# Optimization experiments

Measured on AMD Instinct MI355X. Metric: run time of the kernel, lower is better.

Reference implementation:

```python
import jax, jax.numpy as jnp
import numpy as np

K = 3; STRIDE = 1; PAD = 1; DIL = 1  # from init_kwargs, groups=1


def setup_inputs() -> dict:
    key = jax.random.key(0)
    k1, k2, k3, k4, k5 = jax.random.split(key, 5)
    x = jax.random.normal(k1, (4, 64, 128, 128), dtype=jnp.float32)
    # small offset-conv weights so predicted offsets stay in a realistic few-pixel range
    w_off = jax.random.normal(k2, (2 * K * K, 64, K, K), dtype=jnp.float32) * 0.01
    b_off = jax.random.normal(k3, (2 * K * K,), dtype=jnp.float32) * 0.01
    w = jax.random.normal(k4, (64, 64, K, K), dtype=jnp.float32) * (1.0 / np.sqrt(64 * K * K))
    b = jax.random.normal(k5, (64,), dtype=jnp.float32) * 0.01
    return {"x": x, "w_off": w_off, "b_off": b_off, "w": w, "b": b}


def _conv2d(x, w, b):
    out = jax.lax.conv_general_dilated(
        x, w, window_strides=(STRIDE, STRIDE), padding=((PAD, PAD), (PAD, PAD)),
        rhs_dilation=(DIL, DIL), dimension_numbers=("NCHW", "OIHW", "NCHW"))
    return out + b[None, :, None, None]


def _deform_sample(x, oy, ox):
    # x: [B,C,H,W]; oy/ox: [B,K2,Ho,Wo] learned offsets (y,x)
    B, C, H, W = x.shape
    K2, Ho, Wo = oy.shape[1], oy.shape[2], oy.shape[3]
    k_idx = jnp.arange(K2)
    kh = (k_idx // K).astype(jnp.float32)
    kw = (k_idx % K).astype(jnp.float32)
    base_y = kh[:, None] * DIL + (jnp.arange(Ho, dtype=jnp.float32) * STRIDE - PAD)[None, :]  # [K2,Ho]
    base_x = kw[:, None] * DIL + (jnp.arange(Wo, dtype=jnp.float32) * STRIDE - PAD)[None, :]  # [K2,Wo]
    y = base_y[None, :, :, None] + oy  # [B,K2,Ho,Wo]
    xp = base_x[None, :, None, :] + ox
    y0f = jnp.floor(y); x0f = jnp.floor(xp)
    wy = y - y0f; wx = xp - x0f
    y0 = y0f.astype(jnp.int32); x0 = x0f.astype(jnp.int32)
    imgf = x.reshape(B, C, H * W)
    N = K2 * Ho * Wo

    def gather(yi, xi, cw):
        valid = (yi >= 0) & (yi < H) & (xi >= 0) & (xi < W)  # zero padding outside
        yc = jnp.clip(yi, 0, H - 1); xc = jnp.clip(xi, 0, W - 1)
        idx = (yc * W + xc).reshape(B, 1, N)
        g = jnp.take_along_axis(imgf, idx, axis=2)  # [B,C,N]
        m = (cw * valid.astype(cw.dtype)).reshape(B, 1, N)
        return g * m

    acc = gather(y0, x0, (1 - wy) * (1 - wx))
    acc = acc + gather(y0, x0 + 1, (1 - wy) * wx)
    acc = acc + gather(y0 + 1, x0, wy * (1 - wx))
    acc = acc + gather(y0 + 1, x0 + 1, wy * wx)
    return acc.reshape(B, C, K2, Ho, Wo)


def reference(x, w_off, b_off, w, b):
    # offset-predicting conv (standard conv2d)
    off = _conv2d(x, w_off, b_off)  # [B, 2*K*K, Ho, Wo]
    B = off.shape[0]; Ho, Wo = off.shape[2], off.shape[3]
    off = off.reshape(B, K * K, 2, Ho, Wo)
    oy, ox = off[:, :, 0], off[:, :, 1]
    sampled = _deform_sample(x, oy, ox)  # [B,C,K2,Ho,Wo]
    O = w.shape[0]
    out = jnp.einsum("bckhw,ock->bohw", sampled, w.reshape(O, w.shape[1], K * K))
    return out + b[None, :, None, None]
```

## Files before the change

### kernel.cpp

```cpp
#include <hip/hip_runtime.h>


typedef unsigned short u16;
typedef __attribute__((ext_vector_type(8))) short bf16x8;
typedef __attribute__((ext_vector_type(4))) float f32x4;
#define MFMA __builtin_amdgcn_mfma_f32_16x16x32_bf16

__device__ __forceinline__ void bsplit(float v, u16& h, u16& l) {
  unsigned u = __float_as_uint(v);
  unsigned hb = (u + 0x7fffu + ((u >> 16) & 1u)) & 0xffff0000u;
  h = (u16)(hb >> 16);
  float r = v - __uint_as_float(hb);
  unsigned u2 = __float_as_uint(r);
  l = (u16)((u2 + 0x7fffu + ((u2 >> 16) & 1u)) >> 16);
}

__device__ __forceinline__ u16 brnd(float v) {
  unsigned u = __float_as_uint(v);
  return (u16)((u + 0x7fffu + ((u >> 16) & 1u)) >> 16);
}

__global__ __launch_bounds__(256) void prep_weights(
    const float* __restrict__ w, const float* __restrict__ w_off,
    u16* __restrict__ whi, u16* __restrict__ wlo,
    u16* __restrict__ wofh, u16* __restrict__ wofl) {
  int t = blockIdx.x * 256 + threadIdx.x;
  int stride = gridDim.x * 256;
  for (int i = t; i < 9 * 64 * 64; i += stride) {
    int tap = i >> 12, o = (i >> 6) & 63, c = i & 63;
    u16 h, l;
    bsplit(w[o * 576 + c * 9 + tap], h, l);
    whi[i] = h; wlo[i] = l;
  }
  for (int i = t; i < 9 * 32 * 64; i += stride) {
    int tap = i >> 11, ch = (i >> 6) & 31, c = i & 63;
    float v = (ch < 18) ? w_off[ch * 576 + c * 9 + tap] : 0.f;
    u16 h, l;
    bsplit(v, h, l);
    wofh[i] = h; wofl[i] = l;
  }
}

__global__ __launch_bounds__(256) void transpose_x(
    const float* __restrict__ x, float* __restrict__ xt) {
  __shared__ float tile[64][65];
  int blk = blockIdx.x;
  int wchunk = blk & 1;
  int h = (blk >> 1) & 127;
  int b = blk >> 8;
  int w0 = wchunk * 64;
  int r = threadIdx.x >> 6;
  int lane = threadIdx.x & 63;
#pragma unroll
  for (int i = 0; i < 16; i++) {
    int c = r + i * 4;
    tile[c][lane] = x[(((size_t)(b * 64 + c) * 128) + h) * 128 + w0 + lane];
  }
  __syncthreads();
#pragma unroll
  for (int i = 0; i < 16; i++) {
    int wi = r + i * 4;
    xt[(((size_t)(b * 128 + h) * 128) + w0 + wi) * 64 + lane] = tile[lane][wi];
  }
}

__global__ __launch_bounds__(256) void offset_conv(
    const float* __restrict__ xt, const u16* __restrict__ wofh,
    const u16* __restrict__ wofl, const float* __restrict__ b_off,
    float* __restrict__ off_pix) {
  int blk = blockIdx.x;
  int h = blk & 127, b = blk >> 7;
  int lane = threadIdx.x & 63, wv = threadIdx.x >> 6;
  int lm = lane & 15, lg = lane >> 4;
  const float* xb = xt + (size_t)b * (128 * 128 * 64);

  f32x4 acc[2][2];
#pragma unroll
  for (int i = 0; i < 2; i++)
#pragma unroll
    for (int j = 0; j < 2; j++) acc[i][j] = (f32x4)0.f;

#pragma unroll 1
  for (int tap = 0; tap < 9; tap++) {
    int ky = tap / 3, kx = tap - ky * 3;
    int y = h + ky - 1;
    if ((unsigned)y >= 128u) continue;
#pragma unroll
    for (int kc = 0; kc < 2; kc++) {
      const u16* ah = wofh + tap * 2048 + lm * 64 + kc * 32 + lg * 8;
      const u16* al = wofl + tap * 2048 + lm * 64 + kc * 32 + lg * 8;
      bf16x8 a0h = *(const bf16x8*)ah;
      bf16x8 a0l = *(const bf16x8*)al;
      bf16x8 a1h = *(const bf16x8*)(ah + 1024);
      bf16x8 a1l = *(const bf16x8*)(al + 1024);
#pragma unroll
      for (int pt = 0; pt < 2; pt++) {
        int xx = wv * 32 + pt * 16 + lm + kx - 1;
        bool valid = (unsigned)xx < 128u;
        int xc = min(max(xx, 0), 127);
        const float* xp = xb + ((size_t)(y * 128 + xc)) * 64 + kc * 32 + lg * 8;
        float4 xa = *(const float4*)xp;
        float4 xd = *(const float4*)(xp + 4);
        if (!valid) { xa = make_float4(0, 0, 0, 0); xd = make_float4(0, 0, 0, 0); }
        bf16x8 bh;
        bh[0] = brnd(xa.x); bh[1] = brnd(xa.y);
        bh[2] = brnd(xa.z); bh[3] = brnd(xa.w);
        bh[4] = brnd(xd.x); bh[5] = brnd(xd.y);
        bh[6] = brnd(xd.z); bh[7] = brnd(xd.w);
        acc[pt][0] = MFMA(a0h, bh, acc[pt][0], 0, 0, 0);
        acc[pt][0] = MFMA(a0l, bh, acc[pt][0], 0, 0, 0);
        acc[pt][1] = MFMA(a1h, bh, acc[pt][1], 0, 0, 0);
        acc[pt][1] = MFMA(a1l, bh, acc[pt][1], 0, 0, 0);
      }
    }
  }

  float4 bo = *(const float4*)(b_off + 4 * lg);
  float b16 = b_off[16], b17 = b_off[17];
#pragma unroll
  for (int pt = 0; pt < 2; pt++) {
    int wc = wv * 32 + pt * 16 + lm;
    size_t base = ((size_t)((b * 128 + h) * 128) + wc) * 18;
    float2 s0 = make_float2(acc[pt][0][0] + bo.x, acc[pt][0][1] + bo.y);
    float2 s1 = make_float2(acc[pt][0][2] + bo.z, acc[pt][0][3] + bo.w);
    *(float2*)(off_pix + base + 4 * lg) = s0;
    *(float2*)(off_pix + base + 4 * lg + 2) = s1;
    if (lg == 0) {
      float2 s2 = make_float2(acc[pt][1][0] + b16, acc[pt][1][1] + b17);
      *(float2*)(off_pix + base + 16) = s2;
    }
  }
}

#define SWZ(p, byt) ((byt) ^ (((p) & 7) << 4))
__global__ __launch_bounds__(256) void dcn_main(
    const float* __restrict__ xt, const float* __restrict__ off_pix,
    const u16* __restrict__ whi, const u16* __restrict__ wlo,
    const float* __restrict__ bias, float* __restrict__ out) {
  __shared__ __align__(16) float cw_lds[576][4];
  __shared__ __align__(16) int   ci_lds[576][4];
  __shared__ __align__(16) u16 shi[64 * 64];

  int blk = blockIdx.x;
  int wg = ((blk & 7) << 7) | (blk >> 3);
  int wc = wg & 1, h = (wg >> 1) & 127, b = wg >> 8;
  int w0 = wc * 64;
  int tid = threadIdx.x, lane = tid & 63, wave = tid >> 6;
  int lm = lane & 15, lg = lane >> 4;
  const float* xbase = xt + (size_t)b * (128 * 128 * 64);
  const float* offbase = off_pix + (size_t)((b * 128 + h) * 128 + w0) * 18;

#pragma unroll 1
  for (int it = tid; it < 576; it += 256) {
    int p = it / 9, k = it - p * 9;
    int ky = k / 3, kx = k - ky * 3;
    float2 o2 = *reinterpret_cast<const float2*>(offbase + p * 18 + 2 * k);
    float yf = (float)(h + ky - 1) + o2.x;
    float xf = (float)(w0 + p + kx - 1) + o2.y;
    float y0f = floorf(yf), x0f = floorf(xf);
    float wy = yf - y0f, wx = xf - x0f;
    int y0 = (int)y0f, x0 = (int)x0f;
    int y1 = y0 + 1, x1 = x0 + 1;
    float w00 = (1.f - wy) * (1.f - wx);
    float w01 = (1.f - wy) * wx;
    float w10 = wy * (1.f - wx);
    float w11 = wy * wx;
    bool vy0 = (unsigned)y0 < 128u, vy1 = (unsigned)y1 < 128u;
    bool vx0 = (unsigned)x0 < 128u, vx1 = (unsigned)x1 < 128u;
    if (!(vy0 && vx0)) w00 = 0.f;
    if (!(vy0 && vx1)) w01 = 0.f;
    if (!(vy1 && vx0)) w10 = 0.f;
    if (!(vy1 && vx1)) w11 = 0.f;
    int y0c = min(max(y0, 0), 127), y1c = min(max(y1, 0), 127);
    int x0c = min(max(x0, 0), 127), x1c = min(max(x1, 0), 127);
    *(float4*)cw_lds[it] = make_float4(w00, w01, w10, w11);
    *(int4*)ci_lds[it] =
        make_int4((y0c * 128 + x0c) * 64, (y0c * 128 + x1c) * 64,
                  (y1c * 128 + x0c) * 64, (y1c * 128 + x1c) * 64);
  }
  __syncthreads();

  f32x4 acc[4];
#pragma unroll
  for (int i = 0; i < 4; i++) acc[i] = (f32x4)0.f;

  float g[16][4];

#pragma unroll
  for (int i = 0; i < 16; i++) {
    int4 ci = *(const int4*)ci_lds[(wave * 16 + i) * 9 + 0];
    g[i][0] = xbase[ci.x + lane];
    g[i][1] = xbase[ci.y + lane];
    g[i][2] = xbase[ci.z + lane];
    g[i][3] = xbase[ci.w + lane];
  }

#pragma unroll 1
  for (int tap = 0; tap < 9; tap++) {
#pragma unroll
    for (int i = 0; i < 16; i++) {
      int p = wave * 16 + i;
      float4 cwv = *(const float4*)cw_lds[p * 9 + tap];
      float v = cwv.x * g[i][0] + cwv.y * g[i][1] +
                cwv.z * g[i][2] + cwv.w * g[i][3];
      int byt = SWZ(p, p * 128 + lane * 2);
      *(u16*)((char*)shi + byt) = brnd(v);
    }
    __syncthreads();

    if (tap < 8) {
#pragma unroll
      for (int i = 0; i < 16; i++) {
        int4 ci = *(const int4*)ci_lds[(wave * 16 + i) * 9 + tap + 1];
        g[i][0] = xbase[ci.x + lane];
        g[i][1] = xbase[ci.y + lane];
        g[i][2] = xbase[ci.z + lane];
        g[i][3] = xbase[ci.w + lane];
      }
    }

    const u16* wh = whi + tap * 4096 + (wave * 16 + lm) * 64 + lg * 8;
    const u16* wl = wlo + tap * 4096 + (wave * 16 + lm) * 64 + lg * 8;
    bf16x8 ah0 = *(const bf16x8*)wh;
    bf16x8 ah1 = *(const bf16x8*)(wh + 32);
    bf16x8 al0 = *(const bf16x8*)wl;
    bf16x8 al1 = *(const bf16x8*)(wl + 32);
#pragma unroll
    for (int pt = 0; pt < 4; pt++) {
      int p = pt * 16 + lm;
      int byt0 = SWZ(p, p * 128 + lg * 16);
      int byt1 = SWZ(p, p * 128 + 64 + lg * 16);
      bf16x8 bh0 = *(const bf16x8*)((char*)shi + byt0);
      bf16x8 bh1 = *(const bf16x8*)((char*)shi + byt1);
      acc[pt] = MFMA(ah0, bh0, acc[pt], 0, 0, 0);
      acc[pt] = MFMA(al0, bh0, acc[pt], 0, 0, 0);
      acc[pt] = MFMA(ah1, bh1, acc[pt], 0, 0, 0);
      acc[pt] = MFMA(al1, bh1, acc[pt], 0, 0, 0);
    }
    __syncthreads();
  }

  float4 bv = *(const float4*)(bias + wave * 16 + 4 * lg);
  size_t ob = ((size_t)(b * 64 + wave * 16 + 4 * lg)) * 16384 + h * 128 + w0;
#pragma unroll
  for (int pt = 0; pt < 4; pt++) {
#pragma unroll
    for (int r = 0; r < 4; r++) {
      float bb = (r == 0) ? bv.x : (r == 1) ? bv.y : (r == 2) ? bv.z : bv.w;
      out[ob + (size_t)r * 16384 + pt * 16 + lm] = acc[pt][r] + bb;
    }
  }
}

extern "C" void kernel_launch(void* const* d_in, const int* in_sizes, int n_in,
                              void* d_out, int out_size, void* d_ws, size_t ws_size,
                              hipStream_t stream) {
  const float* x     = (const float*)d_in[0];
  const float* w_off = (const float*)d_in[1];
  const float* b_off = (const float*)d_in[2];
  const float* w     = (const float*)d_in[3];
  const float* b     = (const float*)d_in[4];
  float* out = (float*)d_out;
  char* ws = (char*)d_ws;

  u16*   whi     = (u16*)(ws);
  u16*   wlo     = (u16*)(ws + 73728);
  u16*   wofh    = (u16*)(ws + 147456);
  u16*   wofl    = (u16*)(ws + 184320);
  float* xtw     = (float*)(ws + 221184);
  float* off_pix = (float*)(ws + 16998400);

  prep_weights<<<64, 256, 0, stream>>>(w, w_off, whi, wlo, wofh, wofl);
  transpose_x<<<1024, 256, 0, stream>>>(x, xtw);
  offset_conv<<<512, 256, 0, stream>>>(xtw, wofh, wofl, b_off, off_pix);
  dcn_main<<<1024, 256, 0, stream>>>(xtw, off_pix, whi, wlo, b, out);
}
```

Before: 169.1 us.

## Fuse offset conv into deformable main kernel and merge prep with transpose

Moves the offset-predicting convolution into the main deformable-conv kernel: each workgroup computes the offsets for its 64 pixels with MFMA and keeps them in LDS instead of writing them to and reading them back from global memory. Weight preparation and the x transpose are merged into one launch, so the pipeline goes from four kernel launches to two. The cost is more LDS and registers per workgroup in the main kernel, which may lower occupancy, plus a serial offset phase ahead of sampling inside each block.

```diff
diff --git a/kernel.cpp b/kernel.cpp
--- a/kernel.cpp
+++ b/kernel.cpp
@@ -20,85 +20,89 @@
   return (u16)((u + 0x7fffu + ((u >> 16) & 1u)) >> 16);
 }
 
-__global__ __launch_bounds__(256) void prep_weights(
-    const float* __restrict__ w, const float* __restrict__ w_off,
+__global__ __launch_bounds__(256) void prep_and_transpose(
+    const float* __restrict__ x, const float* __restrict__ w,
+    const float* __restrict__ w_off, float* __restrict__ xt,
     u16* __restrict__ whi, u16* __restrict__ wlo,
     u16* __restrict__ wofh, u16* __restrict__ wofl) {
-  int t = blockIdx.x * 256 + threadIdx.x;
-  int stride = gridDim.x * 256;
-  for (int i = t; i < 9 * 64 * 64; i += stride) {
-    int tap = i >> 12, o = (i >> 6) & 63, c = i & 63;
-    u16 h, l;
-    bsplit(w[o * 576 + c * 9 + tap], h, l);
-    whi[i] = h; wlo[i] = l;
-  }
-  for (int i = t; i < 9 * 32 * 64; i += stride) {
-    int tap = i >> 11, ch = (i >> 6) & 31, c = i & 63;
-    float v = (ch < 18) ? w_off[ch * 576 + c * 9 + tap] : 0.f;
-    u16 h, l;
-    bsplit(v, h, l);
-    wofh[i] = h; wofl[i] = l;
-  }
-}
-
-__global__ __launch_bounds__(256) void transpose_x(
-    const float* __restrict__ x, float* __restrict__ xt) {
   __shared__ float tile[64][65];
   int blk = blockIdx.x;
-  int wchunk = blk & 1;
-  int h = (blk >> 1) & 127;
-  int b = blk >> 8;
-  int w0 = wchunk * 64;
-  int r = threadIdx.x >> 6;
-  int lane = threadIdx.x & 63;
-#pragma unroll
-  for (int i = 0; i < 16; i++) {
-    int c = r + i * 4;
-    tile[c][lane] = x[(((size_t)(b * 64 + c) * 128) + h) * 128 + w0 + lane];
-  }
-  __syncthreads();
-#pragma unroll
-  for (int i = 0; i < 16; i++) {
-    int wi = r + i * 4;
-    xt[(((size_t)(b * 128 + h) * 128) + w0 + wi) * 64 + lane] = tile[lane][wi];
-  }
-}
-
-__global__ __launch_bounds__(256) void offset_conv(
-    const float* __restrict__ xt, const u16* __restrict__ wofh,
-    const u16* __restrict__ wofl, const float* __restrict__ b_off,
-    float* __restrict__ off_pix) {
+  if (blk < 1024) {
+    int wchunk = blk & 1;
+    int h = (blk >> 1) & 127;
+    int b = blk >> 8;
+    int w0 = wchunk * 64;
+    int r = threadIdx.x >> 6;
+    int lane = threadIdx.x & 63;
+#pragma unroll
+    for (int i = 0; i < 16; i++) {
+      int c = r + i * 4;
+      tile[c][lane] = x[(((size_t)(b * 64 + c) * 128) + h) * 128 + w0 + lane];
+    }
+    __syncthreads();
+#pragma unroll
+    for (int i = 0; i < 16; i++) {
+      int wi = r + i * 4;
+      xt[(((size_t)(b * 128 + h) * 128) + w0 + wi) * 64 + lane] = tile[lane][wi];
+    }
+  } else {
+    int t = (blk - 1024) * 256 + threadIdx.x;
+    const int stride = 64 * 256;
+    for (int i = t; i < 9 * 64 * 64; i += stride) {
+      int tap = i >> 12, o = (i >> 6) & 63, c = i & 63;
+      u16 h, l;
+      bsplit(w[o * 576 + c * 9 + tap], h, l);
+      whi[i] = h; wlo[i] = l;
+    }
+    for (int i = t; i < 9 * 32 * 64; i += stride) {
+      int tap = i >> 11, ch = (i >> 6) & 31, c = i & 63;
+      float v = (ch < 18) ? w_off[ch * 576 + c * 9 + tap] : 0.f;
+      u16 h, l;
+      bsplit(v, h, l);
+      wofh[i] = h; wofl[i] = l;
+    }
+  }
+}
+
+#define SWZ(p, byt) ((byt) ^ (((p) & 7) << 4))
+__global__ __launch_bounds__(256) void dcn_fused(
+    const float* __restrict__ xt,
+    const u16* __restrict__ whi, const u16* __restrict__ wlo,
+    const u16* __restrict__ wofh, const u16* __restrict__ wofl,
+    const float* __restrict__ b_off, const float* __restrict__ bias,
+    float* __restrict__ out) {
+  __shared__ __align__(16) float cw_lds[576][4];
+  __shared__ __align__(16) int   ci_lds[576][4];
+  __shared__ __align__(16) u16   shi[64 * 64];
+  __shared__ __align__(16) float offs[64][20];
+
   int blk = blockIdx.x;
-  int h = blk & 127, b = blk >> 7;
-  int lane = threadIdx.x & 63, wv = threadIdx.x >> 6;
+  int wg = ((blk & 7) << 7) | (blk >> 3);
+  int wc = wg & 1, h = (wg >> 1) & 127, b = wg >> 8;
+  int w0 = wc * 64;
+  int tid = threadIdx.x, lane = tid & 63, wave = tid >> 6;
   int lm = lane & 15, lg = lane >> 4;
-  const float* xb = xt + (size_t)b * (128 * 128 * 64);
-
-  f32x4 acc[2][2];
-#pragma unroll
-  for (int i = 0; i < 2; i++)
-#pragma unroll
-    for (int j = 0; j < 2; j++) acc[i][j] = (f32x4)0.f;
-
+  const float* xbase = xt + (size_t)b * (128 * 128 * 64);
+
+  {
+    f32x4 oa0 = (f32x4)0.f, oa1 = (f32x4)0.f;
 #pragma unroll 1
-  for (int tap = 0; tap < 9; tap++) {
-    int ky = tap / 3, kx = tap - ky * 3;
-    int y = h + ky - 1;
-    if ((unsigned)y >= 128u) continue;
-#pragma unroll
-    for (int kc = 0; kc < 2; kc++) {
-      const u16* ah = wofh + tap * 2048 + lm * 64 + kc * 32 + lg * 8;
-      const u16* al = wofl + tap * 2048 + lm * 64 + kc * 32 + lg * 8;
-      bf16x8 a0h = *(const bf16x8*)ah;
-      bf16x8 a0l = *(const bf16x8*)al;
-      bf16x8 a1h = *(const bf16x8*)(ah + 1024);
-      bf16x8 a1l = *(const bf16x8*)(al + 1024);
-#pragma unroll
-      for (int pt = 0; pt < 2; pt++) {
-        int xx = wv * 32 + pt * 16 + lm + kx - 1;
+    for (int tap = 0; tap < 9; tap++) {
+      int ky = tap / 3, kx = tap - ky * 3;
+      int y = h + ky - 1;
+      if ((unsigned)y >= 128u) continue;
+#pragma unroll
+      for (int kc = 0; kc < 2; kc++) {
+        const u16* ah = wofh + tap * 2048 + lm * 64 + kc * 32 + lg * 8;
+        const u16* al = wofl + tap * 2048 + lm * 64 + kc * 32 + lg * 8;
+        bf16x8 a0h = *(const bf16x8*)ah;
+        bf16x8 a0l = *(const bf16x8*)al;
+        bf16x8 a1h = *(const bf16x8*)(ah + 1024);
+        bf16x8 a1l = *(const bf16x8*)(al + 1024);
+        int xx = w0 + wave * 16 + lm + kx - 1;
         bool valid = (unsigned)xx < 128u;
-        int xc = min(max(xx, 0), 127);
-        const float* xp = xb + ((size_t)(y * 128 + xc)) * 64 + kc * 32 + lg * 8;
+        int xcl = min(max(xx, 0), 127);
+        const float* xp = xbase + ((size_t)(y * 128 + xcl)) * 64 + kc * 32 + lg * 8;
         float4 xa = *(const float4*)xp;
         float4 xd = *(const float4*)(xp + 4);
         if (!valid) { xa = make_float4(0, 0, 0, 0); xd = make_float4(0, 0, 0, 0); }
@@ -107,56 +111,33 @@
         bh[2] = brnd(xa.z); bh[3] = brnd(xa.w);
         bh[4] = brnd(xd.x); bh[5] = brnd(xd.y);
         bh[6] = brnd(xd.z); bh[7] = brnd(xd.w);
-        acc[pt][0] = MFMA(a0h, bh, acc[pt][0], 0, 0, 0);
-        acc[pt][0] = MFMA(a0l, bh, acc[pt][0], 0, 0, 0);
-        acc[pt][1] = MFMA(a1h, bh, acc[pt][1], 0, 0, 0);
-        acc[pt][1] = MFMA(a1l, bh, acc[pt][1], 0, 0, 0);
+        oa0 = MFMA(a0h, bh, oa0, 0, 0, 0);
+        oa0 = MFMA(a0l, bh, oa0, 0, 0, 0);
+        oa1 = MFMA(a1h, bh, oa1, 0, 0, 0);
+        oa1 = MFMA(a1l, bh, oa1, 0, 0, 0);
       }
     }
-  }
-
-  float4 bo = *(const float4*)(b_off + 4 * lg);
-  float b16 = b_off[16], b17 = b_off[17];
-#pragma unroll
-  for (int pt = 0; pt < 2; pt++) {
-    int wc = wv * 32 + pt * 16 + lm;
-    size_t base = ((size_t)((b * 128 + h) * 128) + wc) * 18;
-    float2 s0 = make_float2(acc[pt][0][0] + bo.x, acc[pt][0][1] + bo.y);
-    float2 s1 = make_float2(acc[pt][0][2] + bo.z, acc[pt][0][3] + bo.w);
-    *(float2*)(off_pix + base + 4 * lg) = s0;
-    *(float2*)(off_pix + base + 4 * lg + 2) = s1;
+    int px = wave * 16 + lm;
+    float4 bo = *(const float4*)(b_off + 4 * lg);
+    offs[px][4 * lg + 0] = oa0[0] + bo.x;
+    offs[px][4 * lg + 1] = oa0[1] + bo.y;
+    offs[px][4 * lg + 2] = oa0[2] + bo.z;
+    offs[px][4 * lg + 3] = oa0[3] + bo.w;
     if (lg == 0) {
-      float2 s2 = make_float2(acc[pt][1][0] + b16, acc[pt][1][1] + b17);
-      *(float2*)(off_pix + base + 16) = s2;
-    }
-  }
-}
-
-#define SWZ(p, byt) ((byt) ^ (((p) & 7) << 4))
-__global__ __launch_bounds__(256) void dcn_main(
-    const float* __restrict__ xt, const float* __restrict__ off_pix,
-    const u16* __restrict__ whi, const u16* __restrict__ wlo,
-    const float* __restrict__ bias, float* __restrict__ out) {
-  __shared__ __align__(16) float cw_lds[576][4];
-  __shared__ __align__(16) int   ci_lds[576][4];
-  __shared__ __align__(16) u16 shi[64 * 64];
-
-  int blk = blockIdx.x;
-  int wg = ((blk & 7) << 7) | (blk >> 3);
-  int wc = wg & 1, h = (wg >> 1) & 127, b = wg >> 8;
-  int w0 = wc * 64;
-  int tid = threadIdx.x, lane = tid & 63, wave = tid >> 6;
-  int lm = lane & 15, lg = lane >> 4;
-  const float* xbase = xt + (size_t)b * (128 * 128 * 64);
-  const float* offbase = off_pix + (size_t)((b * 128 + h) * 128 + w0) * 18;
+      offs[px][16] = oa1[0] + b_off[16];
+      offs[px][17] = oa1[1] + b_off[17];
+    }
+  }
+  __syncthreads();
 
 #pragma unroll 1
   for (int it = tid; it < 576; it += 256) {
     int p = it / 9, k = it - p * 9;
     int ky = k / 3, kx = k - ky * 3;
-    float2 o2 = *reinterpret_cast<const float2*>(offbase + p * 18 + 2 * k);
-    float yf = (float)(h + ky - 1) + o2.x;
-    float xf = (float)(w0 + p + kx - 1) + o2.y;
+    float oy = offs[p][2 * k];
+    float ox = offs[p][2 * k + 1];
+    float yf = (float)(h + ky - 1) + oy;
+    float xf = (float)(w0 + p + kx - 1) + ox;
     float y0f = floorf(yf), x0f = floorf(xf);
     float wy = yf - y0f, wx = xf - x0f;
     int y0 = (int)y0f, x0 = (int)x0f;
@@ -263,15 +244,12 @@
   float* out = (float*)d_out;
   char* ws = (char*)d_ws;
 
-  u16*   whi     = (u16*)(ws);
-  u16*   wlo     = (u16*)(ws + 73728);
-  u16*   wofh    = (u16*)(ws + 147456);
-  u16*   wofl    = (u16*)(ws + 184320);
-  float* xtw     = (float*)(ws + 221184);
-  float* off_pix = (float*)(ws + 16998400);
-
-  prep_weights<<<64, 256, 0, stream>>>(w, w_off, whi, wlo, wofh, wofl);
-  transpose_x<<<1024, 256, 0, stream>>>(x, xtw);
-  offset_conv<<<512, 256, 0, stream>>>(xtw, wofh, wofl, b_off, off_pix);
-  dcn_main<<<1024, 256, 0, stream>>>(xtw, off_pix, whi, wlo, b, out);
-}
+  u16*   whi  = (u16*)(ws);
+  u16*   wlo  = (u16*)(ws + 73728);
+  u16*   wofh = (u16*)(ws + 147456);
+  u16*   wofl = (u16*)(ws + 184320);
+  float* xtw  = (float*)(ws + 221184);
+
+  prep_and_transpose<<<1088, 256, 0, stream>>>(x, w, w_off, xtw, whi, wlo, wofh, wofl);
+  dcn_fused<<<1024, 256, 0, stream>>>(xtw, whi, wlo, wofh, wofl, b_off, b, out);
+}
```

Result: slower. 184.0 us (+8.8%).

## Keep gathered samples in registers as MFMA B operands and merge prep kernels

Applied to the files above, without the earlier changes.

In the deformable-conv main kernel, the work split changes: each lane now owns one pixel and gathers 16 contiguous channels per bilinear corner with float4 loads. The bilinear combine happens in registers and is packed directly into bf16 MFMA B fragments, so the LDS staging buffer and both per-tap __syncthreads are gone. Each wave now computes all four output-channel tiles for its 16 pixels, loading weights per tile, and gathers for the next tap are software-pipelined behind the current tap's MFMAs. Separately, the weight-prep and transpose kernels are merged into one launch. The costs are more vector registers held live and more repeated weight loads from global memory.

```diff
diff --git a/kernel.cpp b/kernel.cpp
--- a/kernel.cpp
+++ b/kernel.cpp
@@ -20,47 +20,47 @@
   return (u16)((u + 0x7fffu + ((u >> 16) & 1u)) >> 16);
 }
 
-__global__ __launch_bounds__(256) void prep_weights(
-    const float* __restrict__ w, const float* __restrict__ w_off,
+__global__ __launch_bounds__(256) void prep_and_transpose(
+    const float* __restrict__ x, const float* __restrict__ w,
+    const float* __restrict__ w_off, float* __restrict__ xt,
     u16* __restrict__ whi, u16* __restrict__ wlo,
     u16* __restrict__ wofh, u16* __restrict__ wofl) {
-  int t = blockIdx.x * 256 + threadIdx.x;
-  int stride = gridDim.x * 256;
-  for (int i = t; i < 9 * 64 * 64; i += stride) {
-    int tap = i >> 12, o = (i >> 6) & 63, c = i & 63;
-    u16 h, l;
-    bsplit(w[o * 576 + c * 9 + tap], h, l);
-    whi[i] = h; wlo[i] = l;
-  }
-  for (int i = t; i < 9 * 32 * 64; i += stride) {
-    int tap = i >> 11, ch = (i >> 6) & 31, c = i & 63;
-    float v = (ch < 18) ? w_off[ch * 576 + c * 9 + tap] : 0.f;
-    u16 h, l;
-    bsplit(v, h, l);
-    wofh[i] = h; wofl[i] = l;
-  }
-}
-
-__global__ __launch_bounds__(256) void transpose_x(
-    const float* __restrict__ x, float* __restrict__ xt) {
   __shared__ float tile[64][65];
   int blk = blockIdx.x;
-  int wchunk = blk & 1;
-  int h = (blk >> 1) & 127;
-  int b = blk >> 8;
-  int w0 = wchunk * 64;
-  int r = threadIdx.x >> 6;
-  int lane = threadIdx.x & 63;
-#pragma unroll
-  for (int i = 0; i < 16; i++) {
-    int c = r + i * 4;
-    tile[c][lane] = x[(((size_t)(b * 64 + c) * 128) + h) * 128 + w0 + lane];
-  }
-  __syncthreads();
-#pragma unroll
-  for (int i = 0; i < 16; i++) {
-    int wi = r + i * 4;
-    xt[(((size_t)(b * 128 + h) * 128) + w0 + wi) * 64 + lane] = tile[lane][wi];
+  if (blk < 1024) {
+    int wchunk = blk & 1;
+    int h = (blk >> 1) & 127;
+    int b = blk >> 8;
+    int w0 = wchunk * 64;
+    int r = threadIdx.x >> 6;
+    int lane = threadIdx.x & 63;
+#pragma unroll
+    for (int i = 0; i < 16; i++) {
+      int c = r + i * 4;
+      tile[c][lane] = x[(((size_t)(b * 64 + c) * 128) + h) * 128 + w0 + lane];
+    }
+    __syncthreads();
+#pragma unroll
+    for (int i = 0; i < 16; i++) {
+      int wi = r + i * 4;
+      xt[(((size_t)(b * 128 + h) * 128) + w0 + wi) * 64 + lane] = tile[lane][wi];
+    }
+  } else {
+    int t = (blk - 1024) * 256 + threadIdx.x;
+    const int stride = 64 * 256;
+    for (int i = t; i < 9 * 64 * 64; i += stride) {
+      int tap = i >> 12, o = (i >> 6) & 63, c = i & 63;
+      u16 h, l;
+      bsplit(w[o * 576 + c * 9 + tap], h, l);
+      whi[i] = h; wlo[i] = l;
+    }
+    for (int i = t; i < 9 * 32 * 64; i += stride) {
+      int tap = i >> 11, ch = (i >> 6) & 31, c = i & 63;
+      float v = (ch < 18) ? w_off[ch * 576 + c * 9 + tap] : 0.f;
+      u16 h, l;
+      bsplit(v, h, l);
+      wofh[i] = h; wofl[i] = l;
+    }
   }
 }
 
@@ -132,14 +132,12 @@
   }
 }
 
-#define SWZ(p, byt) ((byt) ^ (((p) & 7) << 4))
 __global__ __launch_bounds__(256) void dcn_main(
     const float* __restrict__ xt, const float* __restrict__ off_pix,
     const u16* __restrict__ whi, const u16* __restrict__ wlo,
     const float* __restrict__ bias, float* __restrict__ out) {
   __shared__ __align__(16) float cw_lds[576][4];
   __shared__ __align__(16) int   ci_lds[576][4];
-  __shared__ __align__(16) u16 shi[64 * 64];
 
   int blk = blockIdx.x;
   int wg = ((blk & 7) << 7) | (blk >> 3);
@@ -180,76 +178,94 @@
   }
   __syncthreads();
 
+  int px9 = (wave * 16 + lm) * 9;
+  int cA = lg * 8;
+  int cB = 32 + lg * 8;
+
   f32x4 acc[4];
 #pragma unroll
   for (int i = 0; i < 4; i++) acc[i] = (f32x4)0.f;
 
-  float g[16][4];
-
-#pragma unroll
-  for (int i = 0; i < 16; i++) {
-    int4 ci = *(const int4*)ci_lds[(wave * 16 + i) * 9 + 0];
-    g[i][0] = xbase[ci.x + lane];
-    g[i][1] = xbase[ci.y + lane];
-    g[i][2] = xbase[ci.z + lane];
-    g[i][3] = xbase[ci.w + lane];
-  }
-
+  float4 cor[16];
+  bf16x8 b0, b1;
+
+#define GATHER(T)                                                         \
+  {                                                                       \
+    int4 ci = *(const int4*)ci_lds[px9 + (T)];                            \
+    const float* p0 = xbase + ci.x;                                       \
+    const float* p1 = xbase + ci.y;                                       \
+    const float* p2 = xbase + ci.z;                                       \
+    const float* p3 = xbase + ci.w;                                       \
+    cor[0]  = *(const float4*)(p0 + cA); cor[1]  = *(const float4*)(p0 + cA + 4); \
+    cor[2]  = *(const float4*)(p0 + cB); cor[3]  = *(const float4*)(p0 + cB + 4); \
+    cor[4]  = *(const float4*)(p1 + cA); cor[5]  = *(const float4*)(p1 + cA + 4); \
+    cor[6]  = *(const float4*)(p1 + cB); cor[7]  = *(const float4*)(p1 + cB + 4); \
+    cor[8]  = *(const float4*)(p2 + cA); cor[9]  = *(const float4*)(p2 + cA + 4); \
+    cor[10] = *(const float4*)(p2 + cB); cor[11] = *(const float4*)(p2 + cB + 4); \
+    cor[12] = *(const float4*)(p3 + cA); cor[13] = *(const float4*)(p3 + cA + 4); \
+    cor[14] = *(const float4*)(p3 + cB); cor[15] = *(const float4*)(p3 + cB + 4); \
+  }
+
+#define COMBINE(T)                                                        \
+  {                                                                       \
+    float4 cwv = *(const float4*)cw_lds[px9 + (T)];                       \
+    float v[16];                                                          \
+    _Pragma("unroll")                                                     \
+    for (int q = 0; q < 4; q++) {                                         \
+      const float* c0 = (const float*)&cor[q];                            \
+      const float* c1 = (const float*)&cor[4 + q];                        \
+      const float* c2 = (const float*)&cor[8 + q];                        \
+      const float* c3 = (const float*)&cor[12 + q];                       \
+      _Pragma("unroll")                                                   \
+      for (int j = 0; j < 4; j++)                                         \
+        v[q * 4 + j] = cwv.x * c0[j] + cwv.y * c1[j] +                    \
+                       cwv.z * c2[j] + cwv.w * c3[j];                     \
+    }                                                                     \
+    _Pragma("unroll")                                                     \
+    for (int j = 0; j < 8; j++) { b0[j] = brnd(v[j]); b1[j] = brnd(v[8 + j]); } \
+  }
+
+#define MFMAPHASE(T)                                                      \
+  {                                                                       \
+    _Pragma("unroll")                                                     \
+    for (int ot = 0; ot < 4; ot++) {                                      \
+      const u16* wh = whi + (T) * 4096 + (ot * 16 + lm) * 64 + lg * 8;    \
+      const u16* wl = wlo + (T) * 4096 + (ot * 16 + lm) * 64 + lg * 8;    \
+      bf16x8 ah0 = *(const bf16x8*)wh;                                    \
+      bf16x8 ah1 = *(const bf16x8*)(wh + 32);                             \
+      bf16x8 al0 = *(const bf16x8*)wl;                                    \
+      bf16x8 al1 = *(const bf16x8*)(wl + 32);                             \
+      acc[ot] = MFMA(ah0, b0, acc[ot], 0, 0, 0);                          \
+      acc[ot] = MFMA(al0, b0, acc[ot], 0, 0, 0);                          \
+      acc[ot] = MFMA(ah1, b1, acc[ot], 0, 0, 0);                          \
+      acc[ot] = MFMA(al1, b1, acc[ot], 0, 0, 0);                          \
+    }                                                                     \
+  }
+
+  GATHER(0);
+  COMBINE(0);
 #pragma unroll 1
-  for (int tap = 0; tap < 9; tap++) {
-#pragma unroll
-    for (int i = 0; i < 16; i++) {
-      int p = wave * 16 + i;
-      float4 cwv = *(const float4*)cw_lds[p * 9 + tap];
-      float v = cwv.x * g[i][0] + cwv.y * g[i][1] +
-                cwv.z * g[i][2] + cwv.w * g[i][3];
-      int byt = SWZ(p, p * 128 + lane * 2);
-      *(u16*)((char*)shi + byt) = brnd(v);
-    }
-    __syncthreads();
-
-    if (tap < 8) {
-#pragma unroll
-      for (int i = 0; i < 16; i++) {
-        int4 ci = *(const int4*)ci_lds[(wave * 16 + i) * 9 + tap + 1];
-        g[i][0] = xbase[ci.x + lane];
-        g[i][1] = xbase[ci.y + lane];
-        g[i][2] = xbase[ci.z + lane];
-        g[i][3] = xbase[ci.w + lane];
-      }
-    }
-
-    const u16* wh = whi + tap * 4096 + (wave * 16 + lm) * 64 + lg * 8;
-    const u16* wl = wlo + tap * 4096 + (wave * 16 + lm) * 64 + lg * 8;
-    bf16x8 ah0 = *(const bf16x8*)wh;
-    bf16x8 ah1 = *(const bf16x8*)(wh + 32);
-    bf16x8 al0 = *(const bf16x8*)wl;
-    bf16x8 al1 = *(const bf16x8*)(wl + 32);
-#pragma unroll
-    for (int pt = 0; pt < 4; pt++) {
-      int p = pt * 16 + lm;
-      int byt0 = SWZ(p, p * 128 + lg * 16);
-      int byt1 = SWZ(p, p * 128 + 64 + lg * 16);
-      bf16x8 bh0 = *(const bf16x8*)((char*)shi + byt0);
-      bf16x8 bh1 = *(const bf16x8*)((char*)shi + byt1);
-      acc[pt] = MFMA(ah0, bh0, acc[pt], 0, 0, 0);
-      acc[pt] = MFMA(al0, bh0, acc[pt], 0, 0, 0);
-      acc[pt] = MFMA(ah1, bh1, acc[pt], 0, 0, 0);
-      acc[pt] = MFMA(al1, bh1, acc[pt], 0, 0, 0);
-    }
-    __syncthreads();
-  }
-
-  float4 bv = *(const float4*)(bias + wave * 16 + 4 * lg);
-  size_t ob = ((size_t)(b * 64 + wave * 16 + 4 * lg)) * 16384 + h * 128 + w0;
-#pragma unroll
-  for (int pt = 0; pt < 4; pt++) {
+  for (int t = 0; t < 8; ++t) {
+    GATHER(t + 1);
+    MFMAPHASE(t);
+    COMBINE(t + 1);
+  }
+  MFMAPHASE(8);
+
+#pragma unroll
+  for (int ot = 0; ot < 4; ot++) {
+    float4 bv = *(const float4*)(bias + ot * 16 + 4 * lg);
+    size_t ob = ((size_t)(b * 64 + ot * 16 + 4 * lg)) * 16384 + h * 128 + w0 +
+                wave * 16 + lm;
 #pragma unroll
     for (int r = 0; r < 4; r++) {
       float bb = (r == 0) ? bv.x : (r == 1) ? bv.y : (r == 2) ? bv.z : bv.w;
-      out[ob + (size_t)r * 16384 + pt * 16 + lm] = acc[pt][r] + bb;
-    }
-  }
+      out[ob + (size_t)r * 16384] = acc[ot][r] + bb;
+    }
+  }
+#undef GATHER
+#undef COMBINE
+#undef MFMAPHASE
 }
 
 extern "C" void kernel_launch(void* const* d_in, const int* in_sizes, int n_in,
@@ -270,8 +286,7 @@
   float* xtw     = (float*)(ws + 221184);
   float* off_pix = (float*)(ws + 16998400);
 
-  prep_weights<<<64, 256, 0, stream>>>(w, w_off, whi, wlo, wofh, wofl);
-  transpose_x<<<1024, 256, 0, stream>>>(x, xtw);
+  prep_and_transpose<<<1088, 256, 0, stream>>>(x, w, w_off, xtw, whi, wlo, wofh, wofl);
   offset_conv<<<512, 256, 0, stream>>>(xtw, wofh, wofl, b_off, off_pix);
   dcn_main<<<1024, 256, 0, stream>>>(xtw, off_pix, whi, wlo, b, out);
 }
```

Measured after the change: 238.5 us. 41.1% more time.
